# Performance work log

Measured on AMD Instinct MI355X. Metric: run time of the kernel, lower is better.

The kernel has to match this reference:

```python
import jax, jax.numpy as jnp
import numpy as np

LN_EPS = 1e-5

def _linear(x, w, b):
    return x @ w.T + b

def _layernorm(x, g, b):
    mu = jnp.mean(x, axis=-1, keepdims=True)
    var = jnp.var(x, axis=-1, keepdims=True)
    return (x - mu) * jax.lax.rsqrt(var + LN_EPS) * g + b

def _depthwise_conv1d(x, w):
    # x: [B, S, D], w: [D, 1, 3] (torch layout), padding=1, groups=D, no bias
    xc = jnp.swapaxes(x, 1, 2)  # [B, D, S]
    y = jax.lax.conv_general_dilated(
        xc, w, window_strides=(1,), padding=[(1, 1)],
        dimension_numbers=('NCH', 'OIH', 'NCH'),
        feature_group_count=w.shape[0])
    return jnp.swapaxes(y, 1, 2)

def _ssm(x, A, B, C):
    # h_t = h_{t-1} A^T + x_t B^T ; y_t = h_t C^T
    bsz = x.shape[0]
    h0 = jnp.zeros((bsz, A.shape[0]), dtype=x.dtype)
    def step(h, xt):  # xt: [B, D]
        h = h @ A.T + xt @ B.T
        return h, h @ C.T
    _, ys = jax.lax.scan(step, h0, jnp.swapaxes(x, 0, 1))  # [S, B, D]
    return jnp.swapaxes(ys, 0, 1)

def setup_inputs() -> dict:
    key = jax.random.key(0)
    d_model, d_state, expand = 1024, 64, 2
    B, S = 4, 2048
    ks = jax.random.split(key, 16)
    sm = 1.0 / np.sqrt(d_model)
    inp = {
        'x': jax.random.normal(ks[0], (B, S, d_model), jnp.float32),
        'w1_w': jax.random.normal(ks[1], (d_model, d_model), jnp.float32) * sm,
        'w1_b': jnp.zeros((d_model,), jnp.float32),
        'v1_w': jax.random.normal(ks[2], (d_model, d_model), jnp.float32) * sm,
        'v1_b': jnp.zeros((d_model,), jnp.float32),
        'w2_w': jax.random.normal(ks[3], (d_model, d_model), jnp.float32) * sm,
        'w2_b': jnp.zeros((d_model,), jnp.float32),
        'conv_w': jax.random.normal(ks[4], (d_model, 1, 3), jnp.float32) * (1.0 / np.sqrt(3.0)),
        'A': jax.random.normal(ks[5], (d_state, d_state), jnp.float32) * 0.05,  # spectral radius ~0.4, stable scan
        'Bm': jax.random.normal(ks[6], (d_state, d_model), jnp.float32) * sm,
        'Cm': jax.random.normal(ks[7], (d_model, d_state), jnp.float32) * (1.0 / np.sqrt(d_state)),
        'ln1_g': jnp.ones((d_model,), jnp.float32),
        'ln1_b': jnp.zeros((d_model,), jnp.float32),
        'ln2_g': jnp.ones((d_model,), jnp.float32),
        'ln2_b': jnp.zeros((d_model,), jnp.float32),
        'ff1_w': jax.random.normal(ks[8], (expand * d_model, d_model), jnp.float32) * sm,
        'ff1_b': jnp.zeros((expand * d_model,), jnp.float32),
        'ff2_w': jax.random.normal(ks[9], (d_model, expand * d_model), jnp.float32) * (1.0 / np.sqrt(expand * d_model)),
        'ff2_b': jnp.zeros((d_model,), jnp.float32),
    }
    return inp

def reference(x, w1_w, w1_b, v1_w, v1_b, w2_w, w2_b, conv_w, A, Bm, Cm,
              ln1_g, ln1_b, ln2_g, ln2_b, ff1_w, ff1_b, ff2_w, ff2_b):
    residual = x
    h = _layernorm(x, ln1_g, ln1_b)
    # Mamba block
    x1 = _linear(h, w1_w, w1_b)
    xc = jax.nn.silu(_depthwise_conv1d(x1, conv_w))
    x_ssm = _ssm(xc, A, Bm, Cm)
    v = jax.nn.silu(_linear(h, v1_w, v1_b))
    h = _linear(x_ssm * v, w2_w, w2_b)
    x = h + residual
    residual = x
    h = _layernorm(x, ln2_g, ln2_b)
    h = _linear(jax.nn.gelu(_linear(h, ff1_w, ff1_b), approximate=False), ff2_w, ff2_b)
    return h + residual
```

## Files before the change

### kernel.cpp

```cpp
#include <hip/hip_runtime.h>
#include <hip/hip_bf16.h>

typedef unsigned short u16;
typedef __bf16 bf16x8 __attribute__((ext_vector_type(8)));
typedef float f32x4 __attribute__((ext_vector_type(4)));

#define DEV __device__ __forceinline__

DEV u16 f2bf(float f) {
  __hip_bfloat16 h = __float2bfloat16(f);
  union { __hip_bfloat16 h; u16 u; } c; c.h = h; return c.u;
}
DEV float bf2f(u16 u) {
  unsigned int x = ((unsigned int)u) << 16; float f;
  __builtin_memcpy(&f, &x, 4); return f;
}
DEV float silu_f(float x) { return x / (1.f + __expf(-x)); }
DEV float gelu_f(float x) { return 0.5f * x * (1.f + erff(x * 0.70710678118654752f)); }

DEV void gl_lds16(const void* g, void* l) {
  __builtin_amdgcn_global_load_lds(
      (const __attribute__((address_space(1))) void*)g,
      (__attribute__((address_space(3))) void*)l, 16, 0, 0);
}

template<int N> DEV void vmwait() {
  static_assert(N == 0 || N == 2 || N == 4, "unsupported vmcnt");
  if constexpr (N == 0)      asm volatile("s_waitcnt vmcnt(0)" ::: "memory");
  else if constexpr (N == 2) asm volatile("s_waitcnt vmcnt(2)" ::: "memory");
  else                       asm volatile("s_waitcnt vmcnt(4)" ::: "memory");
}

template<int BM, int EPI>
__global__ __launch_bounds__(512, 2)
void gemm256(const u16* __restrict__ A, const u16* __restrict__ Bw,
             const float* __restrict__ bias, const float* __restrict__ bias2,
             const float* __restrict__ resp,
             void* __restrict__ outp, void* __restrict__ outp2,
             int M, int N, int K)
{
  constexpr int WROWS = BM / 2;
  constexpr int MR = WROWS / 16;
  constexpr int NR = 4;
  constexpr int LA = BM / 64;
  constexpr int LB = 4;
  constexpr int AE = BM * 64;
  constexpr int BUFE = AE + 16384;
  __shared__ alignas(16) u16 lds[2 * BUFE];

  const int t = threadIdx.x;
  const int w = t >> 6, l = t & 63;
  const int wm = w >> 2, wn = w & 3;
  const int lr = l & 15, lq = l >> 4;

  const int nwg = gridDim.x;
  int lin = blockIdx.x;
  if ((nwg & 7) == 0) lin = (lin & 7) * (nwg >> 3) + (lin >> 3);
  const int nbx = N >> 8;
  const int by = lin / nbx, bx = lin - by * nbx;
  const int brow = by * BM, bcol = bx << 8;

  const int ir = l >> 3, ik = l & 7;
  const int kkl = ik ^ ir;
  const u16* gsA[LA];
  const u16* gsB[LB];
#pragma unroll
  for (int s = 0; s < LA; ++s)
    gsA[s] = A + (size_t)(brow + (w * LA + s) * 8 + ir) * K + kkl * 8;
#pragma unroll
  for (int s = 0; s < LB; ++s)
    gsB[s] = Bw + (size_t)(bcol + (w * LB + s) * 8 + ir) * K + kkl * 8;

  auto stageA = [&](int buf) {
#pragma unroll
    for (int s = 0; s < LA; ++s) {
      gl_lds16(gsA[s], &lds[buf * BUFE + (w * LA + s) * 512]);
      gsA[s] += 64;
    }
  };
  auto stageB = [&](int buf) {
#pragma unroll
    for (int s = 0; s < LB; ++s) {
      gl_lds16(gsB[s], &lds[buf * BUFE + AE + (w * LB + s) * 512]);
      gsB[s] += 64;
    }
  };

  f32x4 acc[MR][NR] = {};

  auto kstep = [&](int buf, int ks) {
    bf16x8 af[MR], bfr[NR];
#pragma unroll
    for (int mi = 0; mi < MR; ++mi) {
      const int ro = wm * WROWS + mi * 16 + lr;
      const int ck = (ks * 4 + lq) ^ (ro & 7);
      af[mi] = *(const bf16x8*)&lds[buf * BUFE + ro * 64 + ck * 8];
    }
#pragma unroll
    for (int ni = 0; ni < NR; ++ni) {
      const int ro = wn * 64 + ni * 16 + lr;
      const int ck = (ks * 4 + lq) ^ (ro & 7);
      bfr[ni] = *(const bf16x8*)&lds[buf * BUFE + AE + ro * 64 + ck * 8];
    }
    __builtin_amdgcn_s_setprio(1);
#pragma unroll
    for (int mi = 0; mi < MR; ++mi)
#pragma unroll
      for (int ni = 0; ni < NR; ++ni)
        acc[mi][ni] = __builtin_amdgcn_mfma_f32_16x16x32_bf16(af[mi], bfr[ni], acc[mi][ni], 0, 0, 0);
    __builtin_amdgcn_s_setprio(0);
  };

  stageA(0); stageB(0);
  const int nt = K >> 6;
  int cur = 0;
  for (int kt = 0; kt < nt; ++kt) {
    const int nxt = cur ^ 1;
    if (kt + 1 < nt) { stageA(nxt); vmwait<LA>(); }
    else             { vmwait<0>(); }
    __builtin_amdgcn_s_barrier();
    kstep(cur, 0);
    if (kt + 1 < nt) stageB(nxt);
    kstep(cur, 1);
    __builtin_amdgcn_s_barrier();
    cur = nxt;
  }

#pragma unroll
  for (int ni = 0; ni < NR; ++ni) {
    const int col = bcol + wn * 64 + ni * 16 + lr;
    float bv = 0.f;
    if (EPI == 3 || EPI == 4) bv = bias[col];
    if (EPI == 5) bv = (col < 1024) ? bias[col] : bias2[col - 1024];
#pragma unroll
    for (int mi = 0; mi < MR; ++mi) {
      const int row0 = brow + wm * WROWS + mi * 16 + lq * 4;
#pragma unroll
      for (int r = 0; r < 4; ++r) {
        const int row = row0 + r;
        const float raw = acc[mi][ni][r];
        if (EPI == 3) {
          const size_t idx = (size_t)row * N + col;
          ((float*)outp)[idx] = raw + bv + resp[idx];
        } else if (EPI == 4) {
          ((u16*)outp)[(size_t)row * N + col] = f2bf(gelu_f(raw + bv));
        } else {
          if (col < 1024) ((u16*)outp)[(size_t)row * 1024 + col] = f2bf(raw + bv);
          else ((u16*)outp2)[(size_t)row * 1024 + (col - 1024)] = f2bf(silu_f(raw + bv));
        }
      }
    }
  }
}

template<int EPI>
__global__ __launch_bounds__(256)
void gemm_bt(const u16* __restrict__ A, const u16* __restrict__ Bw,
             const float* __restrict__ bias, const u16* __restrict__ mulp,
             void* __restrict__ outp, int M, int N, int K)
{
  __shared__ u16 As[2][128 * 32];
  __shared__ u16 Bs[2][128 * 32];
  const int t = threadIdx.x;
  const int w = t >> 6, l = t & 63;
  const int wr = w >> 1, wc = w & 1;
  const int brow = blockIdx.y << 7;
  const int bcol = blockIdx.x << 7;

  const u16* gA0 = A + (size_t)(brow + (t >> 2)) * K + ((t & 3) << 3);
  const u16* gA1 = gA0 + (size_t)64 * K;
  int bn0 = bcol + (t >> 2);      if (bn0 > N - 1) bn0 = N - 1;
  int bn1 = bcol + 64 + (t >> 2); if (bn1 > N - 1) bn1 = N - 1;
  const u16* gB0 = Bw + (size_t)bn0 * K + ((t & 3) << 3);
  const u16* gB1 = Bw + (size_t)bn1 * K + ((t & 3) << 3);
  const int woff = w << 9;

  auto stage = [&](int b) {
    gl_lds16(gA0, &As[b][woff]);        gl_lds16(gA1, &As[b][2048 + woff]);
    gl_lds16(gB0, &Bs[b][woff]);        gl_lds16(gB1, &Bs[b][2048 + woff]);
    gA0 += 32; gA1 += 32; gB0 += 32; gB1 += 32;
  };

  f32x4 acc[4][4] = {};
  const int lr = l & 15, lk = (l >> 4) << 3;
  const int nt = K >> 5;

  stage(0);
  __syncthreads();
  int cur = 0;
  for (int kt = 0; kt < nt; ++kt) {
    if (kt + 1 < nt) stage(cur ^ 1);
    bf16x8 af[4], bfr[4];
#pragma unroll
    for (int i = 0; i < 4; ++i)
      af[i] = *(const bf16x8*)&As[cur][(wr * 64 + i * 16 + lr) * 32 + lk];
#pragma unroll
    for (int j = 0; j < 4; ++j)
      bfr[j] = *(const bf16x8*)&Bs[cur][(wc * 64 + j * 16 + lr) * 32 + lk];
    __builtin_amdgcn_s_setprio(1);
#pragma unroll
    for (int i = 0; i < 4; ++i)
#pragma unroll
      for (int j = 0; j < 4; ++j)
        acc[i][j] = __builtin_amdgcn_mfma_f32_16x16x32_bf16(af[i], bfr[j], acc[i][j], 0, 0, 0);
    __builtin_amdgcn_s_setprio(0);
    __syncthreads();
    cur ^= 1;
  }

  const int lq = l >> 4;
#pragma unroll
  for (int j = 0; j < 4; ++j) {
    const int col = bcol + wc * 64 + j * 16 + lr;
    if (col >= N) continue;
    const float bv = (EPI == 0 && bias) ? bias[col] : 0.f;
#pragma unroll
    for (int i = 0; i < 4; ++i) {
      const int row0 = brow + wr * 64 + i * 16 + lq * 4;
#pragma unroll
      for (int r = 0; r < 4; ++r) {
        const size_t idx = (size_t)(row0 + r) * N + col;
        const float raw = acc[i][j][r];
        if (EPI == 0) ((float*)outp)[idx] = raw + bv;
        else          ((u16*)outp)[idx]   = f2bf(raw * bf2f(mulp[idx]));
      }
    }
  }
}

__global__ __launch_bounds__(256)
void ln_bf16(const float* __restrict__ x, const float* __restrict__ g,
             const float* __restrict__ b, u16* __restrict__ out)
{
  const int row = blockIdx.x;
  const int t = threadIdx.x;
  const float4 v = ((const float4*)(x + (size_t)row * 1024))[t];
  float s = v.x + v.y + v.z + v.w;
  float sq = v.x * v.x + v.y * v.y + v.z * v.z + v.w * v.w;
#pragma unroll
  for (int o = 32; o; o >>= 1) { s += __shfl_xor(s, o); sq += __shfl_xor(sq, o); }
  __shared__ float ls[8];
  const int w = t >> 6, l = t & 63;
  if (l == 0) { ls[w] = s; ls[4 + w] = sq; }
  __syncthreads();
  s = ls[0] + ls[1] + ls[2] + ls[3];
  sq = ls[4] + ls[5] + ls[6] + ls[7];
  const float mean = s * (1.f / 1024.f);
  const float var = sq * (1.f / 1024.f) - mean * mean;
  const float rs = rsqrtf(var + 1e-5f);
  const float4 gg = ((const float4*)g)[t];
  const float4 bb = ((const float4*)b)[t];
  ushort4 o;
  o.x = f2bf((v.x - mean) * rs * gg.x + bb.x);
  o.y = f2bf((v.y - mean) * rs * gg.y + bb.y);
  o.z = f2bf((v.z - mean) * rs * gg.z + bb.z);
  o.w = f2bf((v.w - mean) * rs * gg.w + bb.w);
  ((ushort4*)(out + (size_t)row * 1024))[t] = o;
}

__global__ __launch_bounds__(256)
void conv_silu(const u16* __restrict__ x1, const float* __restrict__ cwT,
               u16* __restrict__ xc, int S)
{
  const size_t gid = (size_t)blockIdx.x * 256 + threadIdx.x;
  const int dq = (int)(gid & 255);
  const size_t tok = gid >> 8;
  const int s = (int)(tok % (size_t)S);
  ushort4 zz; zz.x = 0; zz.y = 0; zz.z = 0; zz.w = 0;
  const ushort4* base = (const ushort4*)x1 + tok * 256;
  const ushort4 xm = (s > 0) ? base[dq - 256] : zz;
  const ushort4 x0 = base[dq];
  const ushort4 xp = (s < S - 1) ? base[dq + 256] : zz;
  const float4 w0 = ((const float4*)cwT)[dq];
  const float4 w1 = ((const float4*)(cwT + 1024))[dq];
  const float4 w2 = ((const float4*)(cwT + 2048))[dq];
  ushort4 o;
  o.x = f2bf(silu_f(w0.x * bf2f(xm.x) + w1.x * bf2f(x0.x) + w2.x * bf2f(xp.x)));
  o.y = f2bf(silu_f(w0.y * bf2f(xm.y) + w1.y * bf2f(x0.y) + w2.y * bf2f(xp.y)));
  o.z = f2bf(silu_f(w0.z * bf2f(xm.z) + w1.z * bf2f(x0.z) + w2.z * bf2f(xp.z)));
  o.w = f2bf(silu_f(w0.w * bf2f(xm.w) + w1.w * bf2f(x0.w) + w2.w * bf2f(xp.w)));
  ((ushort4*)xc)[gid] = o;
}

__global__ __launch_bounds__(64)
void ssm_scan(const float* __restrict__ Amat, const float* __restrict__ U,
              u16* __restrict__ H, int S)
{
  const int b = blockIdx.y;
  const int c = blockIdx.x;
  const int j = threadIdx.x;
  const int s0 = c * 32;
  const int tstart = (s0 >= 32) ? (s0 - 32) : 0;
  float4 Ar[16];
#pragma unroll
  for (int q = 0; q < 16; ++q) Ar[q] = ((const float4*)(Amat + j * 64))[q];
  __shared__ float hb[64];
  float h = 0.f;
  const float* Ub = U + (size_t)b * S * 64;
  u16* Hb = H + (size_t)b * S * 64;
  for (int t = tstart; t < s0 + 32; ++t) {
    hb[j] = h;
    __syncthreads();
    float acc0 = Ub[(size_t)t * 64 + j];
#pragma unroll
    for (int q = 0; q < 16; ++q) {
      const float4 hv = *(const float4*)&hb[q * 4];
      acc0 += Ar[q].x * hv.x + Ar[q].y * hv.y + Ar[q].z * hv.z + Ar[q].w * hv.w;
    }
    __syncthreads();
    h = acc0;
    if (t >= s0) Hb[(size_t)t * 64 + j] = f2bf(h);
  }
}

__global__ __launch_bounds__(256)
void cvt_bf16(const float* __restrict__ in, u16* __restrict__ out, int n4)
{
  const int i = blockIdx.x * 256 + threadIdx.x;
  if (i < n4) {
    const float4 v = ((const float4*)in)[i];
    ushort4 o;
    o.x = f2bf(v.x); o.y = f2bf(v.y); o.z = f2bf(v.z); o.w = f2bf(v.w);
    ((ushort4*)out)[i] = o;
  }
}

__global__ __launch_bounds__(256)
void cvt_convw(const float* __restrict__ cw, float* __restrict__ cwT)
{
  const int d = blockIdx.x * 256 + threadIdx.x;
  if (d < 1024) {
    cwT[d]        = cw[d * 3 + 0];
    cwT[1024 + d] = cw[d * 3 + 1];
    cwT[2048 + d] = cw[d * 3 + 2];
  }
}

extern "C" void kernel_launch(void* const* d_in, const int* in_sizes, int n_in,
                              void* d_out, int out_size, void* d_ws, size_t ws_size,
                              hipStream_t stream)
{
  (void)in_sizes; (void)n_in; (void)out_size; (void)ws_size;
  const float* x     = (const float*)d_in[0];
  const float* w1_w  = (const float*)d_in[1];
  const float* w1_b  = (const float*)d_in[2];
  const float* v1_w  = (const float*)d_in[3];
  const float* v1_b  = (const float*)d_in[4];
  const float* w2_w  = (const float*)d_in[5];
  const float* w2_b  = (const float*)d_in[6];
  const float* convw = (const float*)d_in[7];
  const float* Amat  = (const float*)d_in[8];
  const float* Bm    = (const float*)d_in[9];
  const float* Cm    = (const float*)d_in[10];
  const float* ln1_g = (const float*)d_in[11];
  const float* ln1_b = (const float*)d_in[12];
  const float* ln2_g = (const float*)d_in[13];
  const float* ln2_b = (const float*)d_in[14];
  const float* ff1_w = (const float*)d_in[15];
  const float* ff1_b = (const float*)d_in[16];
  const float* ff2_w = (const float*)d_in[17];
  const float* ff2_b = (const float*)d_in[18];

  const int S = 2048, D = 1024, Dff = 2048, NS = 64, BATCH = 4;
  const int NT = BATCH * S;

  char* ws = (char*)d_ws;
  size_t off = 0;
  auto alc = [&](size_t bytes) -> void* {
    void* p = ws + off; off += (bytes + 255) & ~(size_t)255; return p;
  };
  u16*   wb1  = (u16*)alc((size_t)D * D * 2);
  u16*   wv1  = (u16*)alc((size_t)D * D * 2);
  u16*   ww2  = (u16*)alc((size_t)D * D * 2);
  u16*   wf1  = (u16*)alc((size_t)Dff * D * 2);
  u16*   wf2  = (u16*)alc((size_t)D * Dff * 2);
  u16*   wBm  = (u16*)alc((size_t)NS * D * 2);
  u16*   wCm  = (u16*)alc((size_t)D * NS * 2);
  float* cwT  = (float*)alc((size_t)3 * D * 4);
  u16*   h1g  = (u16*)alc((size_t)NT * D * 2);
  u16*   vbuf = (u16*)alc((size_t)NT * D * 2);
  float* Xb   = (float*)alc((size_t)NT * D * 4);
  u16*   xch2 = (u16*)alc((size_t)NT * D * 2);
  float* Ubuf = (float*)alc((size_t)NT * NS * 4);
  u16*   Hbuf = (u16*)alc((size_t)NT * NS * 2);
  u16*   f1b  = (u16*)alc((size_t)NT * Dff * 2);
  u16*   x1b  = (u16*)Xb;

  const dim3 blk(256);
  auto cvt = [&](const float* src, u16* dst, int n) {
    const int n4 = n / 4;
    hipLaunchKernelGGL(cvt_bf16, dim3((n4 + 255) / 256), blk, 0, stream, src, dst, n4);
  };
  cvt(w1_w, wb1, D * D);
  cvt(v1_w, wv1, D * D);
  cvt(w2_w, ww2, D * D);
  cvt(ff1_w, wf1, Dff * D);
  cvt(ff2_w, wf2, D * Dff);
  cvt(Bm, wBm, NS * D);
  cvt(Cm, wCm, D * NS);
  hipLaunchKernelGGL(cvt_convw, dim3(4), blk, 0, stream, convw, cwT);

  hipLaunchKernelGGL(ln_bf16, dim3(NT), blk, 0, stream, x, ln1_g, ln1_b, h1g);
  hipLaunchKernelGGL((gemm256<256, 5>), dim3(256), dim3(512), 0, stream,
                     h1g, wb1, w1_b, v1_b, (const float*)nullptr,
                     (void*)x1b, (void*)vbuf, NT, 2 * D, D);
  hipLaunchKernelGGL(conv_silu, dim3(NT), blk, 0, stream, x1b, cwT, xch2, S);
  hipLaunchKernelGGL((gemm_bt<0>), dim3(1, NT / 128), blk, 0, stream,
                     xch2, wBm, (const float*)nullptr, (const u16*)nullptr,
                     (void*)Ubuf, NT, NS, D);
  hipLaunchKernelGGL(ssm_scan, dim3(S / 32, BATCH), dim3(64), 0, stream,
                     Amat, Ubuf, Hbuf, S);
  hipLaunchKernelGGL((gemm_bt<2>), dim3(D / 128, NT / 128), blk, 0, stream,
                     Hbuf, wCm, (const float*)nullptr, vbuf,
                     (void*)h1g, NT, D, NS);
  hipLaunchKernelGGL((gemm256<128, 3>), dim3(256), dim3(512), 0, stream,
                     h1g, ww2, w2_b, (const float*)nullptr, x,
                     (void*)Xb, (void*)nullptr, NT, D, D);
  hipLaunchKernelGGL(ln_bf16, dim3(NT), blk, 0, stream, Xb, ln2_g, ln2_b, xch2);
  hipLaunchKernelGGL((gemm256<256, 4>), dim3(256), dim3(512), 0, stream,
                     xch2, wf1, ff1_b, (const float*)nullptr, (const float*)nullptr,
                     (void*)f1b, (void*)nullptr, NT, Dff, D);
  hipLaunchKernelGGL((gemm256<128, 3>), dim3(256), dim3(512), 0, stream,
                     f1b, wf2, ff2_b, (const float*)nullptr, Xb,
                     d_out, (void*)nullptr, NT, D, Dff);
}
```

Measured before the change: 302.3 us.

## Restructure GEMM main loop into quarter-tile ping-pong pipeline with deeper prefetch

Rewrites the GEMM k-loop so each 64-wide K tile is processed in four MFMA quarters, with global-to-LDS loads for the next tiles split into halves and interleaved between quarters behind barriers. Prefetch depth increases to roughly two tiles ahead, with explicit vmcnt and lgkmcnt waits. The goal is to hide global load latency and LDS reads behind MFMA work. In exchange it adds many more barriers per iteration, more register-held fragments, and out-of-range tile reloads clamped to the last tile.

```diff
diff --git a/kernel.cpp b/kernel.cpp
--- a/kernel.cpp
+++ b/kernel.cpp
@@ -24,12 +24,14 @@
       (__attribute__((address_space(3))) void*)l, 16, 0, 0);
 }
 
-template<int N> DEV void vmwait() {
-  static_assert(N == 0 || N == 2 || N == 4, "unsupported vmcnt");
+template<int N> DEV void vmwaitN() {
+  static_assert(N == 0 || N == 5 || N == 6, "unsupported vmcnt");
   if constexpr (N == 0)      asm volatile("s_waitcnt vmcnt(0)" ::: "memory");
-  else if constexpr (N == 2) asm volatile("s_waitcnt vmcnt(2)" ::: "memory");
-  else                       asm volatile("s_waitcnt vmcnt(4)" ::: "memory");
-}
+  else if constexpr (N == 5) asm volatile("s_waitcnt vmcnt(5)" ::: "memory");
+  else                       asm volatile("s_waitcnt vmcnt(6)" ::: "memory");
+}
+DEV void lgkm0() { asm volatile("s_waitcnt lgkmcnt(0)" ::: "memory"); }
+DEV void BAR() { __builtin_amdgcn_s_barrier(); }
 
 template<int BM, int EPI>
 __global__ __launch_bounds__(512, 2)
@@ -41,17 +43,21 @@
 {
   constexpr int WROWS = BM / 2;
   constexpr int MR = WROWS / 16;
+  constexpr int MH = MR / 2;
   constexpr int NR = 4;
-  constexpr int LA = BM / 64;
-  constexpr int LB = 4;
+  constexpr int LA = BM / 128;
   constexpr int AE = BM * 64;
-  constexpr int BUFE = AE + 16384;
+  constexpr int BE = 256 * 64;
+  constexpr int BUFE = AE + BE;
+  constexpr int VW = 4 + LA;
   __shared__ alignas(16) u16 lds[2 * BUFE];
 
   const int t = threadIdx.x;
   const int w = t >> 6, l = t & 63;
   const int wm = w >> 2, wn = w & 3;
   const int lr = l & 15, lq = l >> 4;
+  const int ir = l >> 3, ik = l & 7;
+  const int kkl = ik ^ ir;
 
   const int nwg = gridDim.x;
   int lin = blockIdx.x;
@@ -60,71 +66,89 @@
   const int by = lin / nbx, bx = lin - by * nbx;
   const int brow = by * BM, bcol = bx << 8;
 
-  const int ir = l >> 3, ik = l & 7;
-  const int kkl = ik ^ ir;
-  const u16* gsA[LA];
-  const u16* gsB[LB];
-#pragma unroll
-  for (int s = 0; s < LA; ++s)
-    gsA[s] = A + (size_t)(brow + (w * LA + s) * 8 + ir) * K + kkl * 8;
-#pragma unroll
-  for (int s = 0; s < LB; ++s)
-    gsB[s] = Bw + (size_t)(bcol + (w * LB + s) * 8 + ir) * K + kkl * 8;
-
-  auto stageA = [&](int buf) {
-#pragma unroll
-    for (int s = 0; s < LA; ++s) {
-      gl_lds16(gsA[s], &lds[buf * BUFE + (w * LA + s) * 512]);
-      gsA[s] += 64;
-    }
-  };
-  auto stageB = [&](int buf) {
-#pragma unroll
-    for (int s = 0; s < LB; ++s) {
-      gl_lds16(gsB[s], &lds[buf * BUFE + AE + (w * LB + s) * 512]);
-      gsB[s] += 64;
-    }
+  const u16* Ab = A + (size_t)(brow + w * 8 + ir) * K + kkl * 8;
+  const u16* Bb = Bw + (size_t)(bcol + w * 8 + ir) * K + kkl * 8;
+
+  auto stageA = [&](int buf, int h, int kt2) {
+#pragma unroll
+    for (int ld = 0; ld < LA; ++ld)
+      gl_lds16(Ab + (size_t)(h * WROWS + ld * 64) * K + kt2 * 64,
+               &lds[buf * BUFE + (h * WROWS + ld * 64 + w * 8) * 64]);
+  };
+  auto stageB = [&](int buf, int h, int kt2) {
+#pragma unroll
+    for (int ld = 0; ld < 2; ++ld)
+      gl_lds16(Bb + (size_t)(h * 128 + ld * 64) * K + kt2 * 64,
+               &lds[buf * BUFE + AE + (h * 128 + ld * 64 + w * 8) * 64]);
+  };
+
+  bf16x8 afr[MH][2], bfr[NR][2];
+  auto readA = [&](int buf, int q) {
+#pragma unroll
+    for (int mi = 0; mi < MH; ++mi)
+#pragma unroll
+      for (int ks = 0; ks < 2; ++ks) {
+        const int ro = wm * WROWS + (q * MH + mi) * 16 + lr;
+        const int ck = (ks * 4 + lq) ^ (ro & 7);
+        afr[mi][ks] = *(const bf16x8*)&lds[buf * BUFE + ro * 64 + ck * 8];
+      }
+  };
+  auto readB = [&](int buf) {
+#pragma unroll
+    for (int ni = 0; ni < NR; ++ni)
+#pragma unroll
+      for (int ks = 0; ks < 2; ++ks) {
+        const int ro = wn * 64 + ni * 16 + lr;
+        const int ck = (ks * 4 + lq) ^ (ro & 7);
+        bfr[ni][ks] = *(const bf16x8*)&lds[buf * BUFE + AE + ro * 64 + ck * 8];
+      }
   };
 
   f32x4 acc[MR][NR] = {};
-
-  auto kstep = [&](int buf, int ks) {
-    bf16x8 af[MR], bfr[NR];
-#pragma unroll
-    for (int mi = 0; mi < MR; ++mi) {
-      const int ro = wm * WROWS + mi * 16 + lr;
-      const int ck = (ks * 4 + lq) ^ (ro & 7);
-      af[mi] = *(const bf16x8*)&lds[buf * BUFE + ro * 64 + ck * 8];
-    }
-#pragma unroll
-    for (int ni = 0; ni < NR; ++ni) {
-      const int ro = wn * 64 + ni * 16 + lr;
-      const int ck = (ks * 4 + lq) ^ (ro & 7);
-      bfr[ni] = *(const bf16x8*)&lds[buf * BUFE + AE + ro * 64 + ck * 8];
-    }
+  auto mfmaQ = [&](int q, int nh) {
     __builtin_amdgcn_s_setprio(1);
 #pragma unroll
-    for (int mi = 0; mi < MR; ++mi)
-#pragma unroll
-      for (int ni = 0; ni < NR; ++ni)
-        acc[mi][ni] = __builtin_amdgcn_mfma_f32_16x16x32_bf16(af[mi], bfr[ni], acc[mi][ni], 0, 0, 0);
+    for (int mi = 0; mi < MH; ++mi)
+#pragma unroll
+      for (int ni = 0; ni < 2; ++ni)
+#pragma unroll
+        for (int ks = 0; ks < 2; ++ks)
+          acc[q * MH + mi][nh * 2 + ni] = __builtin_amdgcn_mfma_f32_16x16x32_bf16(
+              afr[mi][ks], bfr[nh * 2 + ni][ks], acc[q * MH + mi][nh * 2 + ni], 0, 0, 0);
     __builtin_amdgcn_s_setprio(0);
   };
 
-  stageA(0); stageB(0);
   const int nt = K >> 6;
-  int cur = 0;
+  stageB(0, 0, 0); stageB(0, 1, 0); stageA(0, 0, 0); stageA(0, 1, 0);
+  stageB(1, 0, 1); stageB(1, 1, 1); stageA(1, 0, 1);
+  vmwaitN<VW>();
+  BAR();
+
   for (int kt = 0; kt < nt; ++kt) {
-    const int nxt = cur ^ 1;
-    if (kt + 1 < nt) { stageA(nxt); vmwait<LA>(); }
-    else             { vmwait<0>(); }
-    __builtin_amdgcn_s_barrier();
-    kstep(cur, 0);
-    if (kt + 1 < nt) stageB(nxt);
-    kstep(cur, 1);
-    __builtin_amdgcn_s_barrier();
-    cur = nxt;
-  }
+    const int cur = kt & 1;
+    const int t1 = (kt + 1 < nt) ? kt + 1 : nt - 1;
+    const int t2 = (kt + 2 < nt) ? kt + 2 : nt - 1;
+    readA(cur, 0); readB(cur);
+    stageA(cur ^ 1, 1, t1);
+    BAR(); lgkm0();
+    mfmaQ(0, 0);
+    BAR();
+    stageB(cur, 0, t2);
+    BAR();
+    mfmaQ(0, 1);
+    BAR();
+    readA(cur, 1);
+    stageB(cur, 1, t2);
+    BAR(); lgkm0();
+    mfmaQ(1, 0);
+    BAR();
+    stageA(cur, 0, t2);
+    vmwaitN<VW>();
+    BAR();
+    mfmaQ(1, 1);
+    BAR();
+  }
+  vmwaitN<0>();
 
 #pragma unroll
   for (int ni = 0; ni < NR; ++ni) {
```

New measurement: 304.7 us. Within noise of the previous version (+0.8%).
